# Kernel optimization log

Measured on AMD Instinct MI355X. Metric: run time of the kernel, lower is better.

Reference implementation:

```python
import jax, jax.numpy as jnp
import numpy as np

DIM = 4096
N_HEADS = 32
HEAD_DIM = DIM // N_HEADS
BATCH = 2
SEQ = 1024
THETA = 10000.0
NEG_INF = -1e9


def _rope_cos_sin(seq_len, head_dim):
    # NOTE: original code constructs RotatePosEmbedding with config.dim but applies
    # it per-head; the only shape-consistent interpretation (standard Llama RoPE)
    # uses head_dim frequencies, which is what we implement.
    inv_freq = 1.0 / (THETA ** (jnp.arange(0, head_dim, 2, dtype=jnp.float32) / head_dim))
    angles = jnp.arange(seq_len, dtype=jnp.float32)[:, None] * inv_freq[None, :]  # [S, hd/2]
    return jnp.cos(angles), jnp.sin(angles)


def _apply_rope(x, cos, sin):
    # x: [B,S,H,hd]; rotate consecutive pairs (complex multiply)
    B, S, H, hd = x.shape
    xr = x.reshape(B, S, H, hd // 2, 2)
    x0, x1 = xr[..., 0], xr[..., 1]
    c = cos[None, :, None, :]
    s = sin[None, :, None, :]
    out = jnp.stack([x0 * c - x1 * s, x0 * s + x1 * c], axis=-1)
    return out.reshape(B, S, H, hd)


def setup_inputs() -> dict:
    key = jax.random.key(0)
    ks = jax.random.split(key, 9)
    x = jax.random.normal(ks[0], (BATCH, SEQ, DIM), dtype=jnp.float32)
    scale = 1.0 / np.sqrt(DIM)
    wq = jax.random.normal(ks[1], (DIM, DIM), dtype=jnp.float32) * scale
    wk = jax.random.normal(ks[2], (DIM, DIM), dtype=jnp.float32) * scale
    wv = jax.random.normal(ks[3], (DIM, DIM), dtype=jnp.float32) * scale
    wo = jax.random.normal(ks[4], (DIM, DIM), dtype=jnp.float32) * scale
    bq = jax.random.normal(ks[5], (DIM,), dtype=jnp.float32) * 0.01
    bk = jax.random.normal(ks[6], (DIM,), dtype=jnp.float32) * 0.01
    bv = jax.random.normal(ks[7], (DIM,), dtype=jnp.float32) * 0.01
    bo = jax.random.normal(ks[8], (DIM,), dtype=jnp.float32) * 0.01
    # causal additive mask [S,S]
    mask = jnp.where(jnp.tril(jnp.ones((SEQ, SEQ), dtype=bool)), 0.0, NEG_INF).astype(jnp.float32)
    return {"x": x, "wq": wq, "bq": bq, "wk": wk, "bk": bk, "wv": wv, "bv": bv,
            "wo": wo, "bo": bo, "mask": mask, "start_pos": 0}


def reference(x, wq, bq, wk, bk, wv, bv, wo, bo, mask, start_pos):
    B, S, D = x.shape
    H, hd = N_HEADS, D // N_HEADS
    q = (x @ wq.T + bq).reshape(B, S, H, hd)
    k = (x @ wk.T + bk).reshape(B, S, H, hd)
    v = (x @ wv.T + bv).reshape(B, S, H, hd)
    cos, sin = _rope_cos_sin(S, hd)
    q = _apply_rope(q, cos, sin)
    k = _apply_rope(k, cos, sin)
    # start_pos == 0 prefill: cache slice [:start_pos+S] equals current k/v
    scores = jnp.einsum('bqhd,bkhd->bhqk', q, k) / np.sqrt(hd).astype(np.float32)
    scores = scores + mask[None, None, :, :]
    attn = jax.nn.softmax(scores, axis=-1)
    out = jnp.einsum('bhqk,bkhd->bqhd', attn, v).reshape(B, S, D)
    return out @ wo.T + bo
```

## Files before the change

kernel.cpp:

```cpp
#include <hip/hip_runtime.h>
#include <hip/hip_bf16.h>

#define DIM   4096
#define NH    32
#define HD    128
#define BATCH 2
#define SEQ   1024
#define MROWS (BATCH*SEQ)
#define LDQ   12288

typedef __attribute__((ext_vector_type(8))) short bf16x8;
typedef __attribute__((ext_vector_type(4))) short s16x4;
typedef __attribute__((ext_vector_type(4))) float f32x4;

__device__ inline void gload_lds16(const void* g, void* l) {
  __builtin_amdgcn_global_load_lds(
      (const __attribute__((address_space(1))) void*)g,
      (__attribute__((address_space(3))) void*)l, 16, 0, 0);
}

__device__ inline float bf2f(short b) {
  unsigned u = ((unsigned)(unsigned short)b) << 16;
  return __uint_as_float(u);
}
__device__ inline unsigned short f2bfu(float f) {
  __hip_bfloat16 h = __float2bfloat16(f);
  return *reinterpret_cast<unsigned short*>(&h);
}

__global__ void cvt_bf16_kernel(const float* __restrict__ in,
                                unsigned short* __restrict__ out, long n4) {
  long i = blockIdx.x * (long)blockDim.x + threadIdx.x;
  long stride = (long)gridDim.x * blockDim.x;
  for (; i < n4; i += stride) {
    float4 v = ((const float4*)in)[i];
    ushort4 o;
    o.x = f2bfu(v.x); o.y = f2bfu(v.y); o.z = f2bfu(v.z); o.w = f2bfu(v.w);
    ((ushort4*)out)[i] = o;
  }
}

__global__ void concat3_kernel(const float* __restrict__ a, const float* __restrict__ b,
                               const float* __restrict__ c, float* __restrict__ o) {
  int i = blockIdx.x * blockDim.x + threadIdx.x;
  if (i < 4096) o[i] = a[i];
  else if (i < 8192) o[i] = b[i - 4096];
  else if (i < 12288) o[i] = c[i - 8192];
}

__global__ void rope_table_kernel(float* __restrict__ cosT, float* __restrict__ sinT) {
  int s = blockIdx.x;
  int p = threadIdx.x;
  float inv = powf(10000.0f, -((float)(2 * p)) / 128.0f);
  float a = (float)s * inv;
  cosT[s * 64 + p] = cosf(a);
  sinT[s * 64 + p] = sinf(a);
}

__global__ void reduce_bias_kernel(const float* __restrict__ part,
                                   const float* __restrict__ bias,
                                   float* __restrict__ out) {
  long i = blockIdx.x * (long)blockDim.x + threadIdx.x;
  if (i >= (long)MROWS * DIM / 4) return;
  float4 a = ((const float4*)part)[i];
  float4 b = ((const float4*)(part + (size_t)MROWS * DIM))[i];
  float4 bb = ((const float4*)bias)[(int)(i & (DIM / 4 - 1))];
  float4 o;
  o.x = a.x + b.x + bb.x; o.y = a.y + b.y + bb.y;
  o.z = a.z + b.z + bb.z; o.w = a.w + b.w + bb.w;
  ((float4*)out)[i] = o;
}

template <typename OutT, bool QKV_MODE>
__global__ __launch_bounds__(512, 2) void gemm_hp_kernel(
    const unsigned short* __restrict__ A, const unsigned short* __restrict__ Bw,
    const float* __restrict__ bias, OutT* __restrict__ C,
    int M, int N, int Kstr, int Klen,
    const float* __restrict__ cosT, const float* __restrict__ sinT) {
  __shared__ unsigned short As[4][256 * 32];
  __shared__ unsigned short Bs[4][256 * 32];
  const int t = threadIdx.x;
  const int lane = t & 63;
  const int w = t >> 6;
  const int wm = w >> 2, wn = w & 3;
  const int np = lane & 15, hq = lane >> 4;
  const int kc = ((hq ^ ((np >> 1) & 3)) << 3);

  int bid = blockIdx.y * gridDim.x + blockIdx.x;
  int nwg = gridDim.x * gridDim.y;
  int sb = (bid & 7) * (nwg >> 3) + (bid >> 3);
  int bx = sb % gridDim.x, by = sb / gridDim.x;
  const int m0 = by * 256, n0 = bx * 256;
  const int kb0 = blockIdx.z * Klen;
  const int H = Klen >> 5;
  OutT* Cz = C + (size_t)blockIdx.z * (size_t)M * N;

  auto stage = [&](int slot, int kcol0) {
#pragma unroll
    for (int j = 0; j < 2; ++j) {
      int ci = j * 512 + t;
      int r = ci >> 2, p = ci & 3, g = p ^ ((r >> 1) & 3);
      gload_lds16(A + (size_t)(m0 + r) * Kstr + kcol0 + g * 8, &As[slot][ci * 8]);
    }
#pragma unroll
    for (int j = 0; j < 2; ++j) {
      int ci = j * 512 + t;
      int r = ci >> 2, p = ci & 3, g = p ^ ((r >> 1) & 3);
      gload_lds16(Bw + (size_t)(n0 + r) * Kstr + kcol0 + g * 8, &Bs[slot][ci * 8]);
    }
  };

  stage(0, kb0); stage(1, kb0 + 32); stage(2, kb0 + 64);
  asm volatile("s_waitcnt vmcnt(8)" ::: "memory");
  __builtin_amdgcn_s_barrier();

  f32x4 acc[8][4] = {};

#pragma unroll 1
  for (int h = 0; h < H; ++h) {
    const unsigned short* Asl = As[h & 3];
    const unsigned short* Bsl = Bs[h & 3];
    bf16x8 af[8], bfr[4];
#pragma unroll
    for (int i = 0; i < 8; ++i)
      af[i] = *(const bf16x8*)&Asl[(wm * 128 + i * 16 + np) * 32 + kc];
#pragma unroll
    for (int j = 0; j < 4; ++j)
      bfr[j] = *(const bf16x8*)&Bsl[(wn * 64 + j * 16 + np) * 32 + kc];

    if (h + 3 < H) stage((h + 3) & 3, kb0 + ((h + 3) << 5));

    __builtin_amdgcn_s_setprio(1);
#pragma unroll
    for (int i = 0; i < 8; ++i)
#pragma unroll
      for (int j = 0; j < 4; ++j)
        acc[i][j] = __builtin_amdgcn_mfma_f32_16x16x32_bf16(af[i], bfr[j], acc[i][j], 0, 0, 0);
    __builtin_amdgcn_s_setprio(0);

    if (h + 1 < H) {
      int rem = (h + 2 < H ? 1 : 0) + (h + 3 < H ? 1 : 0);
      if (rem == 2)      asm volatile("s_waitcnt vmcnt(8)" ::: "memory");
      else if (rem == 1) asm volatile("s_waitcnt vmcnt(4)" ::: "memory");
      else               asm volatile("s_waitcnt vmcnt(0)" ::: "memory");
      __builtin_amdgcn_s_barrier();
    }
  }

  const int orow0 = m0 + wm * 128;
  const int ocol0 = n0 + wn * 64 + np;
#pragma unroll
  for (int j = 0; j < 4; ++j) {
    const int col = ocol0 + j * 16;
    float bj = QKV_MODE ? bias[col] : 0.0f;
    const int p0 = (col & 127) >> 1;
    const bool even = (lane & 1) == 0;
    const bool do_rope = QKV_MODE && (col < 8192);
#pragma unroll
    for (int i = 0; i < 8; ++i) {
#pragma unroll
      for (int r = 0; r < 4; ++r) {
        int orow = orow0 + i * 16 + hq * 4 + r;
        float v = acc[i][j][r] + bj;
        float pv = __shfl_xor(v, 1);
        if (do_rope) {
          int srow = orow & (SEQ - 1);
          float c = cosT[srow * 64 + p0];
          float s = sinT[srow * 64 + p0];
          v = even ? (v * c - pv * s) : (pv * s + v * c);
        }
        size_t off = (size_t)orow * N + col;
        if constexpr (sizeof(OutT) == 2)
          ((unsigned short*)Cz)[off] = f2bfu(v);
        else
          ((float*)Cz)[off] = v;
      }
    }
  }
}

__global__ __launch_bounds__(256, 1) void flash_attn_kernel(
    const unsigned short* __restrict__ QKV, unsigned short* __restrict__ O) {
  __shared__ unsigned short Ks[64 * 128];
  __shared__ unsigned short Vt[128 * 64];
  __shared__ unsigned short Ps[4][32 * 64];

  const int p  = blockIdx.x;
  const int bh = blockIdx.y;
  const int b  = bh >> 5;
  const int hh = bh & 31;
  const int t    = threadIdx.x;
  const int lane = t & 63;
  const int w    = t >> 6;
  const int np   = lane & 15;
  const int hq   = lane >> 4;

  const size_t rowbase = (size_t)b * SEQ * LDQ;
  const unsigned short* Qg = QKV + rowbase + (size_t)hh * HD;
  const unsigned short* Kg = QKV + rowbase + 4096 + (size_t)hh * HD;
  const unsigned short* Vg = QKV + rowbase + 8192 + (size_t)hh * HD;
  unsigned short* Og = O + (size_t)b * SEQ * DIM + (size_t)hh * HD;

  const int krow = t >> 2;
  const int kc0  = (t & 3) * 32;
  const int vr0  = (t & 15) * 4;
  const int vc0  = (t >> 4) * 8;

  unsigned short* Pw = &Ps[w][0];
  const float SCALE = 0.08838834764831843f;

  bf16x8 vk[4], vv[4];

#pragma unroll 1
  for (int pass = 0; pass < 2; ++pass) {
    const int qt    = pass ? (7 - p) : p;
    const int nt    = 2 * qt + 2;
    const int qbase = qt * 128 + w * 32;

    bf16x8 qf[2][4];
#pragma unroll
    for (int rb = 0; rb < 2; ++rb)
#pragma unroll
      for (int kb = 0; kb < 4; ++kb)
        qf[rb][kb] = *(const bf16x8*)&Qg[(size_t)(qbase + rb * 16 + np) * LDQ + kb * 32 + hq * 8];

    f32x4 acc[2][8] = {};
    float m_run[2][4], l_run[2][4];
#pragma unroll
    for (int rb = 0; rb < 2; ++rb)
#pragma unroll
      for (int r = 0; r < 4; ++r) { m_run[rb][r] = -3.0e38f; l_run[rb][r] = 0.0f; }

    {
      const unsigned short* kp = Kg + (size_t)krow * LDQ + kc0;
      const unsigned short* vp = Vg + (size_t)vr0 * LDQ + vc0;
#pragma unroll
      for (int jj = 0; jj < 4; ++jj) vk[jj] = *(const bf16x8*)(kp + jj * 8);
#pragma unroll
      for (int jj = 0; jj < 4; ++jj) vv[jj] = *(const bf16x8*)(vp + (size_t)jj * LDQ);
    }

#pragma unroll 1
    for (int kt = 0; kt < nt; ++kt) {
      __syncthreads();

#pragma unroll
      for (int jj = 0; jj < 4; ++jj) {
        int c = (t & 3) * 4 + jj;
        *(bf16x8*)((char*)Ks + krow * 256 + ((c ^ (krow & 7)) << 4)) = vk[jj];
      }
#pragma unroll
      for (int i = 0; i < 8; ++i) {
        int col = vc0 + i;
        s16x4 sv;
        sv[0] = vv[0][i]; sv[1] = vv[1][i]; sv[2] = vv[2][i]; sv[3] = vv[3][i];
        *(s16x4*)((char*)Vt + ((col * 128 + vr0 * 2) ^ ((col & 7) << 4))) = sv;
      }
      __syncthreads();

      if (kt + 1 < nt) {
        const unsigned short* kp = Kg + (size_t)((kt + 1) * 64 + krow) * LDQ + kc0;
        const unsigned short* vp = Vg + (size_t)((kt + 1) * 64 + vr0) * LDQ + vc0;
#pragma unroll
        for (int jj = 0; jj < 4; ++jj) vk[jj] = *(const bf16x8*)(kp + jj * 8);
#pragma unroll
        for (int jj = 0; jj < 4; ++jj) vv[jj] = *(const bf16x8*)(vp + (size_t)jj * LDQ);
      }

      f32x4 sc[4][2] = {};
#pragma unroll
      for (int ct = 0; ct < 4; ++ct) {
#pragma unroll
        for (int kb = 0; kb < 4; ++kb) {
          bf16x8 kf = *(const bf16x8*)((char*)Ks + (ct * 16 + np) * 256 +
                                       (((kb * 4 + hq) ^ (np & 7)) << 4));
          sc[ct][0] = __builtin_amdgcn_mfma_f32_16x16x32_bf16(qf[0][kb], kf, sc[ct][0], 0, 0, 0);
          sc[ct][1] = __builtin_amdgcn_mfma_f32_16x16x32_bf16(qf[1][kb], kf, sc[ct][1], 0, 0, 0);
        }
      }

      const bool maskt = (kt >= 2 * qt);
#pragma unroll
      for (int ct = 0; ct < 4; ++ct) {
        int kvc = kt * 64 + ct * 16 + np;
#pragma unroll
        for (int rb = 0; rb < 2; ++rb)
#pragma unroll
          for (int r = 0; r < 4; ++r) {
            float v = sc[ct][rb][r] * SCALE;
            if (maskt && kvc > qbase + rb * 16 + hq * 4 + r) v = -1.0e9f;
            sc[ct][rb][r] = v;
          }
      }

      float sf[2][4];
#pragma unroll
      for (int rb = 0; rb < 2; ++rb)
#pragma unroll
        for (int r = 0; r < 4; ++r) {
          float tmax = fmaxf(fmaxf(sc[0][rb][r], sc[1][rb][r]),
                             fmaxf(sc[2][rb][r], sc[3][rb][r]));
          tmax = fmaxf(tmax, __shfl_xor(tmax, 1));
          tmax = fmaxf(tmax, __shfl_xor(tmax, 2));
          tmax = fmaxf(tmax, __shfl_xor(tmax, 4));
          tmax = fmaxf(tmax, __shfl_xor(tmax, 8));
          float mn = fmaxf(m_run[rb][r], tmax);
          sf[rb][r] = __expf(m_run[rb][r] - mn);
          m_run[rb][r] = mn;
        }

#pragma unroll
      for (int rb = 0; rb < 2; ++rb)
#pragma unroll
        for (int r = 0; r < 4; ++r) {
          int prow = rb * 16 + hq * 4 + r;
          int swz = (prow & 7) << 4;
          float rsum = 0.f;
#pragma unroll
          for (int ct = 0; ct < 4; ++ct) {
            float pv = __expf(sc[ct][rb][r] - m_run[rb][r]);
            rsum += pv;
            *(unsigned short*)((char*)Pw + ((prow * 128 + (ct * 16 + np) * 2) ^ swz)) = f2bfu(pv);
          }
          rsum += __shfl_xor(rsum, 1);
          rsum += __shfl_xor(rsum, 2);
          rsum += __shfl_xor(rsum, 4);
          rsum += __shfl_xor(rsum, 8);
          l_run[rb][r] = l_run[rb][r] * sf[rb][r] + rsum;
        }

#pragma unroll
      for (int rb = 0; rb < 2; ++rb)
#pragma unroll
        for (int nt2 = 0; nt2 < 8; ++nt2)
#pragma unroll
          for (int r = 0; r < 4; ++r)
            acc[rb][nt2][r] *= sf[rb][r];

#pragma unroll
      for (int kb2 = 0; kb2 < 2; ++kb2) {
        bf16x8 pa0 = *(const bf16x8*)((char*)Pw +
            (((0 * 16 + np) * 128 + kb2 * 64 + hq * 16) ^ ((np & 7) << 4)));
        bf16x8 pa1 = *(const bf16x8*)((char*)Pw +
            (((1 * 16 + np) * 128 + kb2 * 64 + hq * 16) ^ ((np & 7) << 4)));
#pragma unroll
        for (int nt2 = 0; nt2 < 8; ++nt2) {
          int col = nt2 * 16 + np;
          bf16x8 vf = *(const bf16x8*)((char*)Vt +
              ((col * 128 + kb2 * 64 + hq * 16) ^ ((col & 7) << 4)));
          acc[0][nt2] = __builtin_amdgcn_mfma_f32_16x16x32_bf16(pa0, vf, acc[0][nt2], 0, 0, 0);
          acc[1][nt2] = __builtin_amdgcn_mfma_f32_16x16x32_bf16(pa1, vf, acc[1][nt2], 0, 0, 0);
        }
      }
    }

#pragma unroll
    for (int rb = 0; rb < 2; ++rb)
#pragma unroll
      for (int r = 0; r < 4; ++r) {
        float rl = 1.0f / l_run[rb][r];
        int orow = qbase + rb * 16 + hq * 4 + r;
#pragma unroll
        for (int nt2 = 0; nt2 < 8; ++nt2)
          Og[(size_t)orow * DIM + nt2 * 16 + np] = f2bfu(acc[rb][nt2][r] * rl);
      }
  }
}

extern "C" void kernel_launch(void* const* d_in, const int* in_sizes, int n_in,
                              void* d_out, int out_size, void* d_ws, size_t ws_size,
                              hipStream_t stream) {
  const float* x  = (const float*)d_in[0];
  const float* wq = (const float*)d_in[1];
  const float* bq = (const float*)d_in[2];
  const float* wk = (const float*)d_in[3];
  const float* bk = (const float*)d_in[4];
  const float* wv = (const float*)d_in[5];
  const float* bv = (const float*)d_in[6];
  const float* wo = (const float*)d_in[7];
  const float* bo = (const float*)d_in[8];
  float* out = (float*)d_out;

  char* ws = (char*)d_ws;
  unsigned short* wqkvb = (unsigned short*)(ws);
  float* part           = (float*)(ws);
  unsigned short* wob   = (unsigned short*)(ws + (96ll  << 20));
  unsigned short* xb    = (unsigned short*)(ws + (128ll << 20));
  unsigned short* qkv   = (unsigned short*)(ws + (144ll << 20));
  unsigned short* ab    = (unsigned short*)(ws + (192ll << 20));
  float* biasqkv = (float*)(ws + (208ll << 20));
  float* cosT    = (float*)(ws + (208ll << 20) + (64  << 10));
  float* sinT    = (float*)(ws + (208ll << 20) + (320 << 10));

  cvt_bf16_kernel<<<2048, 256, 0, stream>>>(x,  xb, (long)MROWS * DIM / 4);
  cvt_bf16_kernel<<<2048, 256, 0, stream>>>(wq, wqkvb,                        (long)DIM * DIM / 4);
  cvt_bf16_kernel<<<2048, 256, 0, stream>>>(wk, wqkvb + (size_t)DIM * DIM,    (long)DIM * DIM / 4);
  cvt_bf16_kernel<<<2048, 256, 0, stream>>>(wv, wqkvb + 2 * (size_t)DIM * DIM,(long)DIM * DIM / 4);
  cvt_bf16_kernel<<<2048, 256, 0, stream>>>(wo, wob, (long)DIM * DIM / 4);

  concat3_kernel<<<48, 256, 0, stream>>>(bq, bk, bv, biasqkv);
  rope_table_kernel<<<SEQ, 64, 0, stream>>>(cosT, sinT);

  dim3 gq(LDQ / 256, MROWS / 256, 1);
  gemm_hp_kernel<unsigned short, true><<<gq, 512, 0, stream>>>(
      xb, wqkvb, biasqkv, qkv, MROWS, LDQ, DIM, DIM, cosT, sinT);

  dim3 ga(4, BATCH * NH);
  flash_attn_kernel<<<ga, 256, 0, stream>>>(qkv, ab);

  dim3 go(DIM / 256, MROWS / 256, 2);
  gemm_hp_kernel<float, false><<<go, 512, 0, stream>>>(
      ab, wob, nullptr, part, MROWS, DIM, DIM, DIM / 2, nullptr, nullptr);

  reduce_bias_kernel<<<(MROWS * DIM / 4 + 255) / 256, 256, 0, stream>>>(part, bo, out);
}
```

Baseline: 533.8 us.

## Use 128x128 GEMM tiles, drop split-K for output projection, fuse conversions

Replaces the 256x256, 512-thread GEMM with a 128x128, 256-thread variant using a 3-stage LDS pipeline. This gives the projection GEMMs more workgroups to fill the CUs. The output projection no longer uses split-K with a separate reduce+bias kernel: bias is added in the epilogue and results are written straight to the output. The five fp32-to-bf16 conversion launches are merged into one kernel. Smaller tiles lower data reuse per workgroup and raise global/LDS traffic per FLOP, in exchange for better occupancy and fewer launches.

```diff
diff --git a/kernel.cpp b/kernel.cpp
--- a/kernel.cpp
+++ b/kernel.cpp
@@ -28,15 +28,33 @@
   return *reinterpret_cast<unsigned short*>(&h);
 }
 
-__global__ void cvt_bf16_kernel(const float* __restrict__ in,
-                                unsigned short* __restrict__ out, long n4) {
+__global__ void cvt_all_kernel(const float* __restrict__ x, const float* __restrict__ wq,
+                               const float* __restrict__ wk, const float* __restrict__ wv,
+                               const float* __restrict__ wo,
+                               unsigned short* __restrict__ xb,
+                               unsigned short* __restrict__ wqkvb,
+                               unsigned short* __restrict__ wob) {
+  const long NW = 4l << 20;
+  const long NX = 2l << 20;
+  const long total = NX + 4 * NW;
   long i = blockIdx.x * (long)blockDim.x + threadIdx.x;
   long stride = (long)gridDim.x * blockDim.x;
-  for (; i < n4; i += stride) {
-    float4 v = ((const float4*)in)[i];
+  for (; i < total; i += stride) {
+    const float* src; unsigned short* dst; long off;
+    if (i < NX) { src = x; dst = xb; off = i; }
+    else {
+      long j = i - NX;
+      int wsel = (int)(j >> 22);
+      off = j & (NW - 1);
+      if (wsel == 0)      { src = wq; dst = wqkvb; }
+      else if (wsel == 1) { src = wk; dst = wqkvb + (size_t)DIM * DIM; }
+      else if (wsel == 2) { src = wv; dst = wqkvb + 2 * (size_t)DIM * DIM; }
+      else                { src = wo; dst = wob; }
+    }
+    float4 v = ((const float4*)src)[off];
     ushort4 o;
     o.x = f2bfu(v.x); o.y = f2bfu(v.y); o.z = f2bfu(v.z); o.w = f2bfu(v.w);
-    ((ushort4*)out)[i] = o;
+    ((ushort4*)dst)[off] = o;
   }
 }
 
@@ -57,32 +75,18 @@
   sinT[s * 64 + p] = sinf(a);
 }
 
-__global__ void reduce_bias_kernel(const float* __restrict__ part,
-                                   const float* __restrict__ bias,
-                                   float* __restrict__ out) {
-  long i = blockIdx.x * (long)blockDim.x + threadIdx.x;
-  if (i >= (long)MROWS * DIM / 4) return;
-  float4 a = ((const float4*)part)[i];
-  float4 b = ((const float4*)(part + (size_t)MROWS * DIM))[i];
-  float4 bb = ((const float4*)bias)[(int)(i & (DIM / 4 - 1))];
-  float4 o;
-  o.x = a.x + b.x + bb.x; o.y = a.y + b.y + bb.y;
-  o.z = a.z + b.z + bb.z; o.w = a.w + b.w + bb.w;
-  ((float4*)out)[i] = o;
-}
-
-template <typename OutT, bool QKV_MODE>
-__global__ __launch_bounds__(512, 2) void gemm_hp_kernel(
+template <typename OutT, bool ROPE>
+__global__ __launch_bounds__(256, 2) void gemm_m97p_kernel(
     const unsigned short* __restrict__ A, const unsigned short* __restrict__ Bw,
     const float* __restrict__ bias, OutT* __restrict__ C,
-    int M, int N, int Kstr, int Klen,
+    int M, int N, int Kstr,
     const float* __restrict__ cosT, const float* __restrict__ sinT) {
-  __shared__ unsigned short As[4][256 * 32];
-  __shared__ unsigned short Bs[4][256 * 32];
+  __shared__ unsigned short As[3][128 * 32];
+  __shared__ unsigned short Bs[3][128 * 32];
   const int t = threadIdx.x;
   const int lane = t & 63;
   const int w = t >> 6;
-  const int wm = w >> 2, wn = w & 3;
+  const int wm = w >> 1, wn = w & 1;
   const int np = lane & 15, hq = lane >> 4;
   const int kc = ((hq ^ ((np >> 1) & 3)) << 3);
 
@@ -90,74 +94,75 @@
   int nwg = gridDim.x * gridDim.y;
   int sb = (bid & 7) * (nwg >> 3) + (bid >> 3);
   int bx = sb % gridDim.x, by = sb / gridDim.x;
-  const int m0 = by * 256, n0 = bx * 256;
-  const int kb0 = blockIdx.z * Klen;
-  const int H = Klen >> 5;
-  OutT* Cz = C + (size_t)blockIdx.z * (size_t)M * N;
+  const int m0 = by * 128, n0 = bx * 128;
+  const int H = Kstr >> 5;
 
   auto stage = [&](int slot, int kcol0) {
 #pragma unroll
     for (int j = 0; j < 2; ++j) {
-      int ci = j * 512 + t;
+      int ci = j * 256 + t;
       int r = ci >> 2, p = ci & 3, g = p ^ ((r >> 1) & 3);
       gload_lds16(A + (size_t)(m0 + r) * Kstr + kcol0 + g * 8, &As[slot][ci * 8]);
     }
 #pragma unroll
     for (int j = 0; j < 2; ++j) {
-      int ci = j * 512 + t;
+      int ci = j * 256 + t;
       int r = ci >> 2, p = ci & 3, g = p ^ ((r >> 1) & 3);
       gload_lds16(Bw + (size_t)(n0 + r) * Kstr + kcol0 + g * 8, &Bs[slot][ci * 8]);
     }
   };
 
-  stage(0, kb0); stage(1, kb0 + 32); stage(2, kb0 + 64);
-  asm volatile("s_waitcnt vmcnt(8)" ::: "memory");
+  stage(0, 0); stage(1, 32);
+  asm volatile("s_waitcnt vmcnt(4)" ::: "memory");
   __builtin_amdgcn_s_barrier();
 
-  f32x4 acc[8][4] = {};
-
+  f32x4 acc[4][4] = {};
+
+  int sl = 0;
 #pragma unroll 1
-  for (int h = 0; h < H; ++h) {
-    const unsigned short* Asl = As[h & 3];
-    const unsigned short* Bsl = Bs[h & 3];
-    bf16x8 af[8], bfr[4];
-#pragma unroll
-    for (int i = 0; i < 8; ++i)
-      af[i] = *(const bf16x8*)&Asl[(wm * 128 + i * 16 + np) * 32 + kc];
+  for (int u = 0; u < H; ++u) {
+    const unsigned short* Asl = As[sl];
+    const unsigned short* Bsl = Bs[sl];
+    bf16x8 af[4], bfr[4];
+#pragma unroll
+    for (int i = 0; i < 4; ++i)
+      af[i] = *(const bf16x8*)&Asl[(wm * 64 + i * 16 + np) * 32 + kc];
 #pragma unroll
     for (int j = 0; j < 4; ++j)
       bfr[j] = *(const bf16x8*)&Bsl[(wn * 64 + j * 16 + np) * 32 + kc];
 
-    if (h + 3 < H) stage((h + 3) & 3, kb0 + ((h + 3) << 5));
+    if (u + 2 < H) {
+      int ssl = sl + 2; if (ssl >= 3) ssl -= 3;
+      stage(ssl, (u + 2) << 5);
+    }
 
     __builtin_amdgcn_s_setprio(1);
 #pragma unroll
-    for (int i = 0; i < 8; ++i)
+    for (int i = 0; i < 4; ++i)
 #pragma unroll
       for (int j = 0; j < 4; ++j)
         acc[i][j] = __builtin_amdgcn_mfma_f32_16x16x32_bf16(af[i], bfr[j], acc[i][j], 0, 0, 0);
     __builtin_amdgcn_s_setprio(0);
 
-    if (h + 1 < H) {
-      int rem = (h + 2 < H ? 1 : 0) + (h + 3 < H ? 1 : 0);
-      if (rem == 2)      asm volatile("s_waitcnt vmcnt(8)" ::: "memory");
-      else if (rem == 1) asm volatile("s_waitcnt vmcnt(4)" ::: "memory");
-      else               asm volatile("s_waitcnt vmcnt(0)" ::: "memory");
+    if (u + 1 < H) {
+      if (u + 2 < H) asm volatile("s_waitcnt vmcnt(4)" ::: "memory");
+      else           asm volatile("s_waitcnt vmcnt(0)" ::: "memory");
       __builtin_amdgcn_s_barrier();
     }
+    sl = (sl == 2) ? 0 : sl + 1;
   }
 
-  const int orow0 = m0 + wm * 128;
+  const int orow0 = m0 + wm * 64;
   const int ocol0 = n0 + wn * 64 + np;
 #pragma unroll
   for (int j = 0; j < 4; ++j) {
     const int col = ocol0 + j * 16;
-    float bj = QKV_MODE ? bias[col] : 0.0f;
+    float bj = bias[col];
     const int p0 = (col & 127) >> 1;
     const bool even = (lane & 1) == 0;
-    const bool do_rope = QKV_MODE && (col < 8192);
-#pragma unroll
-    for (int i = 0; i < 8; ++i) {
+    const bool do_rope = ROPE && (col < 8192);
+#pragma unroll
+    for (int i = 0; i < 4; ++i) {
 #pragma unroll
       for (int r = 0; r < 4; ++r) {
         int orow = orow0 + i * 16 + hq * 4 + r;
@@ -171,9 +176,9 @@
         }
         size_t off = (size_t)orow * N + col;
         if constexpr (sizeof(OutT) == 2)
-          ((unsigned short*)Cz)[off] = f2bfu(v);
+          ((unsigned short*)C)[off] = f2bfu(v);
         else
-          ((float*)Cz)[off] = v;
+          ((float*)C)[off] = v;
       }
     }
   }
@@ -383,7 +388,6 @@
 
   char* ws = (char*)d_ws;
   unsigned short* wqkvb = (unsigned short*)(ws);
-  float* part           = (float*)(ws);
   unsigned short* wob   = (unsigned short*)(ws + (96ll  << 20));
   unsigned short* xb    = (unsigned short*)(ws + (128ll << 20));
   unsigned short* qkv   = (unsigned short*)(ws + (144ll << 20));
@@ -392,25 +396,19 @@
   float* cosT    = (float*)(ws + (208ll << 20) + (64  << 10));
   float* sinT    = (float*)(ws + (208ll << 20) + (320 << 10));
 
-  cvt_bf16_kernel<<<2048, 256, 0, stream>>>(x,  xb, (long)MROWS * DIM / 4);
-  cvt_bf16_kernel<<<2048, 256, 0, stream>>>(wq, wqkvb,                        (long)DIM * DIM / 4);
-  cvt_bf16_kernel<<<2048, 256, 0, stream>>>(wk, wqkvb + (size_t)DIM * DIM,    (long)DIM * DIM / 4);
-  cvt_bf16_kernel<<<2048, 256, 0, stream>>>(wv, wqkvb + 2 * (size_t)DIM * DIM,(long)DIM * DIM / 4);
-  cvt_bf16_kernel<<<2048, 256, 0, stream>>>(wo, wob, (long)DIM * DIM / 4);
+  cvt_all_kernel<<<4096, 256, 0, stream>>>(x, wq, wk, wv, wo, xb, wqkvb, wob);
 
   concat3_kernel<<<48, 256, 0, stream>>>(bq, bk, bv, biasqkv);
   rope_table_kernel<<<SEQ, 64, 0, stream>>>(cosT, sinT);
 
-  dim3 gq(LDQ / 256, MROWS / 256, 1);
-  gemm_hp_kernel<unsigned short, true><<<gq, 512, 0, stream>>>(
-      xb, wqkvb, biasqkv, qkv, MROWS, LDQ, DIM, DIM, cosT, sinT);
+  dim3 gq(LDQ / 128, MROWS / 128);
+  gemm_m97p_kernel<unsigned short, true><<<gq, 256, 0, stream>>>(
+      xb, wqkvb, biasqkv, qkv, MROWS, LDQ, DIM, cosT, sinT);
 
   dim3 ga(4, BATCH * NH);
   flash_attn_kernel<<<ga, 256, 0, stream>>>(qkv, ab);
 
-  dim3 go(DIM / 256, MROWS / 256, 2);
-  gemm_hp_kernel<float, false><<<go, 512, 0, stream>>>(
-      ab, wob, nullptr, part, MROWS, DIM, DIM, DIM / 2, nullptr, nullptr);
-
-  reduce_bias_kernel<<<(MROWS * DIM / 4 + 255) / 256, 256, 0, stream>>>(part, bo, out);
-}
+  dim3 go(DIM / 128, MROWS / 128);
+  gemm_m97p_kernel<float, false><<<go, 256, 0, stream>>>(
+      ab, wob, bo, out, MROWS, DIM, DIM, nullptr, nullptr);
+}
```

Measured after the change: 534.7 us. Within noise of the previous version (+0.2%).
